# Optimization experiments

Hardware: AMD Instinct MI355X
Metric: run time of the kernel (lower is better)

## Reference

```python
import jax, jax.numpy as jnp
import numpy as np
from jax import lax

R = 3
D = (2 * R + 1) ** 2  # 49 local offsets


def _unfold(x, r):
    # torch F.unfold(kernel=2r+1, padding=r): (B,C,H,W) -> (B, C*K*K, H, W),
    # channel-major (c, ky, kx) ordering, matching conv_general_dilated_patches.
    k = 2 * r + 1
    return lax.conv_general_dilated_patches(
        x, (k, k), (1, 1), [(r, r), (r, r)],
        dimension_numbers=("NCHW", "OIHW", "NCHW"))


def _l2norm(x, eps=1e-12):
    n = jnp.sqrt(jnp.sum(x * x, axis=1, keepdims=True))
    return x / jnp.maximum(n, eps)


def setup_inputs() -> dict:
    key = jax.random.key(0)
    ks = jax.random.split(key, 8)
    B, Cin, Cmid, H, W = 2, 256, 128, 112, 112
    phi_cur = jax.random.normal(ks[0], (B, Cin, H, W), jnp.float32)
    phi_rnd = jax.random.normal(ks[1], (B, Cin, H, W), jnp.float32)
    P_cur = jax.random.normal(ks[2], (B, 3, H, W), jnp.float32)
    P_rnd = jax.random.normal(ks[3], (B, 3, H, W), jnp.float32)
    Wq = jax.random.normal(ks[4], (Cmid, Cin), jnp.float32) * 0.05
    Wk = jax.random.normal(ks[5], (Cmid, Cin), jnp.float32) * 0.05
    Wv = jax.random.normal(ks[6], (D, D), jnp.float32) * 0.1
    bv = jnp.zeros((D,), jnp.float32)
    gamma = jnp.array(1.0, jnp.float32)
    return dict(phi_cur=phi_cur, phi_rnd=phi_rnd, P_cur=P_cur, P_rnd=P_rnd,
                Wq=Wq, Wk=Wk, Wv=Wv, bv=bv, gamma=gamma)


def reference(phi_cur, phi_rnd, P_cur, P_rnd, Wq, Wk, Wv, bv, gamma):
    B, _, H, W = phi_cur.shape
    # 1x1 convs + channel L2 normalize
    q = _l2norm(jnp.einsum('oc,bchw->bohw', Wq, phi_cur))
    k = _l2norm(jnp.einsum('oc,bchw->bohw', Wk, phi_rnd))
    # local cost volume: patches (B, Cmid, D, H, W)
    patches = _unfold(k, R).reshape(B, -1, D, H, W)
    corr = jnp.einsum('bchw,bcdhw->bdhw', q, patches)  # (B,D,H,W)
    vol_corr = jnp.einsum('ed,bdhw->behw', Wv, corr) + bv[None, :, None, None]
    # geometric bias
    Pr = _unfold(P_rnd, R).reshape(B, 3, D, H, W)
    dP = P_cur[:, :, None, :, :] - Pr  # (B,3,D,H,W)
    dz = dP[:, 2]
    dist = jnp.sqrt(jnp.clip(jnp.sum(dP * dP, axis=1), 1e-12, None))
    logits = vol_corr + gamma * (-dist - 0.5 * jnp.abs(dz))
    w = jax.nn.softmax(logits, axis=1)
    off = jnp.arange(-R, R + 1, dtype=w.dtype)
    dY, dX = jnp.meshgrid(off, off, indexing='ij')
    offx = dX.reshape(1, D, 1, 1)
    offy = dY.reshape(1, D, 1, 1)
    du = jnp.sum(w * offx, axis=1, keepdims=True)
    dv = jnp.sum(w * offy, axis=1, keepdims=True)
    conf = jnp.max(w, axis=1, keepdims=True)
    return du, dv, conf
```

## Files before the change

### kernel.cpp

```cpp
#include <hip/hip_runtime.h>
#include <hip/hip_bf16.h>
#include <math.h>

constexpr int B    = 2;
constexpr int CIN  = 256;
constexpr int CMID = 128;
constexpr int H    = 112;
constexpr int W    = 112;
constexpr int HW   = H * W;
constexpr int NPIX = B * HW;
constexpr int RAD  = 3;
constexpr int KS   = 7;
constexpr int DD   = 49;

typedef __attribute__((ext_vector_type(8))) short  short8;
typedef __attribute__((ext_vector_type(4))) float  float4v;

__device__ __forceinline__ unsigned pkbf(float a, float b) {
    __hip_bfloat162 h = __float22bfloat162_rn(make_float2(a, b));
    union { __hip_bfloat162 h2; unsigned u; } c;
    c.h2 = h;
    return c.u;
}

__global__ __launch_bounds__(256) void prep(
    const float* __restrict__ Wq, const float* __restrict__ Wk,
    const float* __restrict__ Wv,
    unsigned short* __restrict__ wqb, unsigned short* __restrict__ wkb,
    float* __restrict__ wvp)
{
    if (blockIdx.x < 64) {
        const int i  = blockIdx.x * 256 + threadIdx.x;
        const int n4 = (CMID * CIN) / 4;
        const float4 v = (i < n4) ? ((const float4*)Wq)[i] : ((const float4*)Wk)[i - n4];
        uint2 r;
        r.x = pkbf(v.x, v.y);
        r.y = pkbf(v.z, v.w);
        if (i < n4) ((uint2*)wqb)[i] = r;
        else        ((uint2*)wkb)[i - n4] = r;
    } else {
        for (int idx = threadIdx.x; idx < DD * 52; idx += 256) {
            const int r = idx / 52, c = idx % 52;
            wvp[idx] = (c < DD) ? Wv[r * DD + c] : 0.f;
        }
    }
}

constexpr int PSTR = 264;

__global__ __launch_bounds__(256, 4) void proj_mfma(
    const float* __restrict__ phi_cur, const float* __restrict__ phi_rnd,
    const unsigned short* __restrict__ wq_bf, const unsigned short* __restrict__ wk_bf,
    unsigned short* __restrict__ q_ws, unsigned short* __restrict__ k_ws)
{
    __shared__ unsigned short pt[64 * PSTR];
    __shared__ float red[4][64];

    const int tid  = threadIdx.x;
    const int lane = tid & 63;
    const int wv   = __builtin_amdgcn_readfirstlane(tid >> 6);
    const int t    = blockIdx.y;

    const float* __restrict__ phi          = t ? phi_rnd : phi_cur;
    const unsigned short* __restrict__ Wbf = t ? wk_bf : wq_bf;
    unsigned short* __restrict__ outp      = t ? k_ws : q_ws;

    const int pgb = blockIdx.x * 64;
    const int b   = pgb / HW;
    const int pim = pgb % HW;
    const float* pbase = phi + (size_t)b * CIN * HW + pim;

    const int m = lane & 15, quad = lane >> 4;

    short8 af[2][8];
#pragma unroll
    for (int ot = 0; ot < 2; ++ot)
#pragma unroll
        for (int kc = 0; kc < 8; ++kc)
            af[ot][kc] = *(const short8*)(Wbf +
                (size_t)(wv * 32 + ot * 16 + m) * CIN + kc * 32 + quad * 8);

#pragma unroll
    for (int half = 0; half < 2; ++half) {
        float4 va[4], vb[4];
#pragma unroll
        for (int p = 0; p < 4; ++p) {
            const int idx = (half * 4 + p) * 256 + tid;
            const int cp  = idx >> 4;
            const int pq  = idx & 15;
            const int c0  = cp * 2;
            va[p] = *(const float4*)(pbase + (size_t)c0 * HW + pq * 4);
            vb[p] = *(const float4*)(pbase + (size_t)(c0 + 1) * HW + pq * 4);
        }
#pragma unroll
        for (int p = 0; p < 4; ++p) {
            const int idx = (half * 4 + p) * 256 + tid;
            const int cp  = idx >> 4;
            const int pq  = idx & 15;
            const int c0  = cp * 2;
            const int swz = ((pq >> 1) & 3) << 3;
            const int col = c0 ^ swz;
            *(unsigned*)(pt + (pq * 4 + 0) * PSTR + col) = pkbf(va[p].x, vb[p].x);
            *(unsigned*)(pt + (pq * 4 + 1) * PSTR + col) = pkbf(va[p].y, vb[p].y);
            *(unsigned*)(pt + (pq * 4 + 2) * PSTR + col) = pkbf(va[p].z, vb[p].z);
            *(unsigned*)(pt + (pq * 4 + 3) * PSTR + col) = pkbf(va[p].w, vb[p].w);
        }
    }

    __syncthreads();

    float4v acc[2][4];
#pragma unroll
    for (int ot = 0; ot < 2; ++ot)
#pragma unroll
        for (int nt = 0; nt < 4; ++nt) acc[ot][nt] = (float4v)0.f;

#pragma unroll
    for (int kc = 0; kc < 8; ++kc) {
        short8 bfr[4];
#pragma unroll
        for (int nt = 0; nt < 4; ++nt) {
            const int row = nt * 16 + m;
            const int col = (kc * 32 + quad * 8) ^ (((row >> 3) & 3) << 3);
            bfr[nt] = *(const short8*)(pt + row * PSTR + col);
        }
#pragma unroll
        for (int nt = 0; nt < 4; ++nt) {
            acc[0][nt] = __builtin_amdgcn_mfma_f32_16x16x32_bf16(af[0][kc], bfr[nt], acc[0][nt], 0, 0, 0);
            acc[1][nt] = __builtin_amdgcn_mfma_f32_16x16x32_bf16(af[1][kc], bfr[nt], acc[1][nt], 0, 0, 0);
        }
    }

#pragma unroll
    for (int nt = 0; nt < 4; ++nt) {
        float ss = 0.f;
#pragma unroll
        for (int ot = 0; ot < 2; ++ot)
#pragma unroll
            for (int r = 0; r < 4; ++r)
                ss = fmaf(acc[ot][nt][r], acc[ot][nt][r], ss);
        ss += __shfl_xor(ss, 16, 64);
        ss += __shfl_xor(ss, 32, 64);
        if (quad == 0) red[wv][nt * 16 + m] = ss;
    }
    __syncthreads();

    float inv[4];
#pragma unroll
    for (int nt = 0; nt < 4; ++nt) {
        const int px = nt * 16 + m;
        const float tot = red[0][px] + red[1][px] + red[2][px] + red[3][px];
        inv[nt] = 1.f / fmaxf(sqrtf(tot), 1e-12f);
    }

#pragma unroll
    for (int nt = 0; nt < 4; ++nt)
#pragma unroll
        for (int ot = 0; ot < 2; ++ot) {
            uint2 st;
            st.x = pkbf(acc[ot][nt][0] * inv[nt], acc[ot][nt][1] * inv[nt]);
            st.y = pkbf(acc[ot][nt][2] * inv[nt], acc[ot][nt][3] * inv[nt]);
            *(uint2*)(outp + (size_t)(pgb + nt * 16 + m) * CMID
                      + wv * 32 + ot * 16 + quad * 4) = st;
        }
}

constexpr int TILE = 16;
constexpr int COLS = TILE + 6;
constexpr int NV   = KS * COLS;
constexpr int KSTR = 136;

__global__ __launch_bounds__(256, 3) void corr_kernel(
    const unsigned short* __restrict__ q_ws, const unsigned short* __restrict__ k_ws,
    const float* __restrict__ P_cur, const float* __restrict__ P_rnd,
    const float* __restrict__ wvp, const float* __restrict__ bv,
    const float* __restrict__ gamma_p, float* __restrict__ out)
{
    __shared__ unsigned short kt[NV * KSTR];
    __shared__ alignas(16) unsigned short qt[TILE * KSTR];
    __shared__ float cs[TILE][52];

    const int tid  = threadIdx.x;
    const int lane = tid & 63;
    const int wv   = __builtin_amdgcn_readfirstlane(tid >> 6);

    const int fid = (blockIdx.z * H + blockIdx.y) * (W / TILE) + blockIdx.x;
    const int swz = (fid & 7) * 196 + (fid >> 3);
    const int b   = swz / (H * (W / TILE));
    const int rem = swz % (H * (W / TILE));
    const int h   = rem / (W / TILE);
    const int w0  = (rem % (W / TILE)) * TILE;

    const int sub  = tid & 15;
    const int vgrp = tid >> 4;
    uint4 stv[10];
#pragma unroll
    for (int pass = 0; pass < 10; ++pass) {
        const int vi = pass * 16 + vgrp;
        uint4 v = make_uint4(0, 0, 0, 0);
        if (vi < NV) {
            const int rr = vi / COLS;
            const int cc = vi % COLS;
            const int hh = h + rr - RAD;
            const int ww = w0 + cc - RAD;
            if (hh >= 0 && hh < H && ww >= 0 && ww < W)
                v = *(const uint4*)(k_ws + (size_t)(b * HW + hh * W + ww) * CMID + sub * 8);
        }
        stv[pass] = v;
    }
    const uint4 qv = *(const uint4*)(q_ws + (size_t)(b * HW + h * W + w0 + vgrp) * CMID + sub * 8);

    const int  ld    = (lane < DD) ? lane : 0;
    const bool valid = (lane < DD);
    float4 wq4[13];
#pragma unroll
    for (int j = 0; j < 13; ++j)
        wq4[j] = *(const float4*)(wvp + ld * 52 + j * 4);
    const float bvv   = bv[ld];
    const float gamma = gamma_p[0];

    const int dy = ld / KS - RAD;
    const int dx = ld % KS - RAD;
    float geo[4];
#pragma unroll
    for (int i = 0; i < 4; ++i) {
        const int pl = wv * 4 + i;
        const int hn = h + dy, wn = w0 + pl + dx;
        const bool inb = valid && hn >= 0 && hn < H && wn >= 0 && wn < W;
        const float* pc = P_cur + (size_t)b * 3 * HW + (h * W + w0 + pl);
        const float cx = pc[0], cy = pc[HW], cz = pc[2 * HW];
        float rx = 0.f, ry = 0.f, rz = 0.f;
        if (inb) {
            const float* pr = P_rnd + (size_t)b * 3 * HW + (hn * W + wn);
            rx = pr[0]; ry = pr[HW]; rz = pr[2 * HW];
        }
        const float dpx = cx - rx, dpy = cy - ry, dpz = cz - rz;
        const float dist = sqrtf(fmaxf(dpx * dpx + dpy * dpy + dpz * dpz, 1e-12f));
        geo[i] = gamma * (-dist - 0.5f * fabsf(dpz));
    }

#pragma unroll
    for (int pass = 0; pass < 10; ++pass) {
        const int vi = pass * 16 + vgrp;
        if (vi < NV)
            *(uint4*)(kt + vi * KSTR + sub * 8) = stv[pass];
    }
    *(uint4*)(qt + vgrp * KSTR + sub * 8) = qv;

    __syncthreads();

    if (tid < TILE * 3)
        cs[tid / 3][49 + tid % 3] = 0.f;

    const int m = lane & 15, quad = lane >> 4;
    short8 aqf[4];
#pragma unroll
    for (int kc = 0; kc < 4; ++kc)
        aqf[kc] = *(const short8*)(qt + m * KSTR + kc * 32 + quad * 8);

    for (int g = wv; g < 14; g += 4) {
        const int r  = g >> 1;
        const int nt = g & 1;
        const int vi = min(r * COLS + nt * 16 + m, NV - 1);
        const short8 b0 = *(const short8*)(kt + vi * KSTR + 0 * 32 + quad * 8);
        const short8 b1 = *(const short8*)(kt + vi * KSTR + 1 * 32 + quad * 8);
        const short8 b2 = *(const short8*)(kt + vi * KSTR + 2 * 32 + quad * 8);
        const short8 b3 = *(const short8*)(kt + vi * KSTR + 3 * 32 + quad * 8);
        float4v a0 = (float4v)0.f, a1 = (float4v)0.f;
        a0 = __builtin_amdgcn_mfma_f32_16x16x32_bf16(aqf[0], b0, a0, 0, 0, 0);
        a1 = __builtin_amdgcn_mfma_f32_16x16x32_bf16(aqf[1], b1, a1, 0, 0, 0);
        a0 = __builtin_amdgcn_mfma_f32_16x16x32_bf16(aqf[2], b2, a0, 0, 0, 0);
        a1 = __builtin_amdgcn_mfma_f32_16x16x32_bf16(aqf[3], b3, a1, 0, 0, 0);
#pragma unroll
        for (int r4 = 0; r4 < 4; ++r4) a0[r4] += a1[r4];
#pragma unroll
        for (int reg = 0; reg < 4; ++reg) {
            const int p   = quad * 4 + reg;
            const int off = nt * 16 + m - p;
            if (off >= 0 && off <= 6)
                cs[p][r * 7 + off] = a0[reg];
        }
    }
    __syncthreads();
    float* lsf = reinterpret_cast<float*>(qt);

#pragma unroll
    for (int i = 0; i < 4; ++i) {
        const int pl = wv * 4 + i;
        float logit = -INFINITY;
        if (valid) {
            float va0 = bvv, va1 = 0.f;
#pragma unroll
            for (int e4 = 0; e4 < 13; ++e4) {
                const float4 c4 = *(const float4*)&cs[pl][e4 * 4];
                const float4 w4 = wq4[e4];
                if (e4 & 1) {
                    va1 = fmaf(w4.x, c4.x, va1);
                    va1 = fmaf(w4.y, c4.y, va1);
                    va1 = fmaf(w4.z, c4.z, va1);
                    va1 = fmaf(w4.w, c4.w, va1);
                } else {
                    va0 = fmaf(w4.x, c4.x, va0);
                    va0 = fmaf(w4.y, c4.y, va0);
                    va0 = fmaf(w4.z, c4.z, va0);
                    va0 = fmaf(w4.w, c4.w, va0);
                }
            }
            logit = (va0 + va1) + geo[i];
        }
        lsf[pl * 64 + lane] = logit;
    }

    {
        const int pli = lane >> 4;
        const int dq  = lane & 15;
        const int pl  = wv * 4 + pli;

        const float4 v = ((const float4*)lsf)[pl * 16 + dq];

        float m4 = fmaxf(fmaxf(v.x, v.y), fmaxf(v.z, v.w));
#pragma unroll
        for (int s = 1; s < 16; s <<= 1)
            m4 = fmaxf(m4, __shfl_xor(m4, s, 64));

        const float e0 = __expf(v.x - m4);
        const float e1 = __expf(v.y - m4);
        const float e2 = __expf(v.z - m4);
        const float e3 = __expf(v.w - m4);
        float Z = (e0 + e1) + (e2 + e3);

        const int c0i = dq * 4;
        float dus = 0.f, dvs = 0.f;
        {
            const float ex[4] = { e0, e1, e2, e3 };
#pragma unroll
            for (int j = 0; j < 4; ++j) {
                const int col = c0i + j;
                dus = fmaf(ex[j], (float)(col % KS - RAD), dus);
                dvs = fmaf(ex[j], (float)(col / KS - RAD), dvs);
            }
        }
#pragma unroll
        for (int s = 1; s < 16; s <<= 1) {
            Z   += __shfl_xor(Z,   s, 64);
            dus += __shfl_xor(dus, s, 64);
            dvs += __shfl_xor(dvs, s, 64);
        }

        if (dq == 0) {
            const int pg = b * HW + h * W + w0 + pl;
            const float invZ = 1.f / Z;
            out[pg]            = dus * invZ;
            out[NPIX + pg]     = dvs * invZ;
            out[2 * NPIX + pg] = invZ;
        }
    }
}

extern "C" void kernel_launch(void* const* d_in, const int* in_sizes, int n_in,
                              void* d_out, int out_size, void* d_ws, size_t ws_size,
                              hipStream_t stream)
{
    const float* phi_cur = (const float*)d_in[0];
    const float* phi_rnd = (const float*)d_in[1];
    const float* P_cur   = (const float*)d_in[2];
    const float* P_rnd   = (const float*)d_in[3];
    const float* Wq      = (const float*)d_in[4];
    const float* Wk      = (const float*)d_in[5];
    const float* Wv      = (const float*)d_in[6];
    const float* bv      = (const float*)d_in[7];
    const float* gm      = (const float*)d_in[8];
    float* out = (float*)d_out;

    unsigned short* ws   = (unsigned short*)d_ws;
    unsigned short* q_ws = ws;
    unsigned short* k_ws = q_ws + (size_t)NPIX * CMID;
    unsigned short* wqb  = k_ws + (size_t)NPIX * CMID;
    unsigned short* wkb  = wqb + (size_t)CMID * CIN;
    float*          wvp  = (float*)(wkb + (size_t)CMID * CIN);

    prep<<<dim3(65), 256, 0, stream>>>(Wq, Wk, Wv, wqb, wkb, wvp);

    proj_mfma<<<dim3(NPIX / 64, 2), 256, 0, stream>>>(
        phi_cur, phi_rnd, wqb, wkb, q_ws, k_ws);

    corr_kernel<<<dim3(W / TILE, H, B), 256, 0, stream>>>(
        q_ws, k_ws, P_cur, P_rnd, wvp, bv, gm, out);
}
```

Baseline: 131.4 us.

## Split projection work by pixel rows per wave to drop block barriers

Each wave now owns 16 pixels across all 128 output channels, loading and transposing only its own pixel rows into shared memory. The L2-norm reduction can then stay inside the wave, which removes both __syncthreads and the shared reduction buffer. Weight fragments are streamed from global memory per k-chunk with a one-step software prefetch instead of being held in registers up front. The cost is that every wave re-reads the whole weight matrix, which raises global and L2 traffic.

```diff
diff --git a/kernel.cpp b/kernel.cpp
--- a/kernel.cpp
+++ b/kernel.cpp
@@ -54,7 +54,6 @@
     unsigned short* __restrict__ q_ws, unsigned short* __restrict__ k_ws)
 {
     __shared__ unsigned short pt[64 * PSTR];
-    __shared__ float red[4][64];
 
     const int tid  = threadIdx.x;
     const int lane = tid & 63;
@@ -71,98 +70,80 @@
     const float* pbase = phi + (size_t)b * CIN * HW + pim;
 
     const int m = lane & 15, quad = lane >> 4;
-
-    short8 af[2][8];
-#pragma unroll
-    for (int ot = 0; ot < 2; ++ot)
-#pragma unroll
-        for (int kc = 0; kc < 8; ++kc)
-            af[ot][kc] = *(const short8*)(Wbf +
-                (size_t)(wv * 32 + ot * 16 + m) * CIN + kc * 32 + quad * 8);
+    const int prow0 = wv * 16;
+
+    const int cpl = lane >> 2;
+    const int pq  = lane & 3;
+    const float* pb2 = pbase + prow0 + pq * 4;
 
 #pragma unroll
     for (int half = 0; half < 2; ++half) {
         float4 va[4], vb[4];
 #pragma unroll
         for (int p = 0; p < 4; ++p) {
-            const int idx = (half * 4 + p) * 256 + tid;
-            const int cp  = idx >> 4;
-            const int pq  = idx & 15;
-            const int c0  = cp * 2;
-            va[p] = *(const float4*)(pbase + (size_t)c0 * HW + pq * 4);
-            vb[p] = *(const float4*)(pbase + (size_t)(c0 + 1) * HW + pq * 4);
+            const int c0 = ((half * 4 + p) * 16 + cpl) * 2;
+            va[p] = *(const float4*)(pb2 + (size_t)c0 * HW);
+            vb[p] = *(const float4*)(pb2 + (size_t)(c0 + 1) * HW);
         }
 #pragma unroll
         for (int p = 0; p < 4; ++p) {
-            const int idx = (half * 4 + p) * 256 + tid;
-            const int cp  = idx >> 4;
-            const int pq  = idx & 15;
-            const int c0  = cp * 2;
-            const int swz = ((pq >> 1) & 3) << 3;
-            const int col = c0 ^ swz;
-            *(unsigned*)(pt + (pq * 4 + 0) * PSTR + col) = pkbf(va[p].x, vb[p].x);
-            *(unsigned*)(pt + (pq * 4 + 1) * PSTR + col) = pkbf(va[p].y, vb[p].y);
-            *(unsigned*)(pt + (pq * 4 + 2) * PSTR + col) = pkbf(va[p].z, vb[p].z);
-            *(unsigned*)(pt + (pq * 4 + 3) * PSTR + col) = pkbf(va[p].w, vb[p].w);
-        }
-    }
-
-    __syncthreads();
-
-    float4v acc[2][4];
-#pragma unroll
-    for (int ot = 0; ot < 2; ++ot)
-#pragma unroll
-        for (int nt = 0; nt < 4; ++nt) acc[ot][nt] = (float4v)0.f;
+            const int c0 = ((half * 4 + p) * 16 + cpl) * 2;
+#pragma unroll
+            for (int j = 0; j < 4; ++j) {
+                const int row = prow0 + pq * 4 + j;
+                const int col = c0 ^ (((row >> 3) & 3) << 3);
+                *(unsigned*)(pt + row * PSTR + col) =
+                    pkbf((&va[p].x)[j], (&vb[p].x)[j]);
+            }
+        }
+    }
+
+    const unsigned short* wrow = Wbf + (size_t)m * CIN + quad * 8;
+    const int brow = prow0 + m;
+    const int bswz = ((brow >> 3) & 3) << 3;
+
+    float4v acc[8];
+#pragma unroll
+    for (int ot = 0; ot < 8; ++ot) acc[ot] = (float4v)0.f;
+
+    short8 afC[8], afN[8];
+#pragma unroll
+    for (int ot = 0; ot < 8; ++ot)
+        afC[ot] = *(const short8*)(wrow + (size_t)ot * 16 * CIN);
 
 #pragma unroll
     for (int kc = 0; kc < 8; ++kc) {
-        short8 bfr[4];
-#pragma unroll
-        for (int nt = 0; nt < 4; ++nt) {
-            const int row = nt * 16 + m;
-            const int col = (kc * 32 + quad * 8) ^ (((row >> 3) & 3) << 3);
-            bfr[nt] = *(const short8*)(pt + row * PSTR + col);
-        }
-#pragma unroll
-        for (int nt = 0; nt < 4; ++nt) {
-            acc[0][nt] = __builtin_amdgcn_mfma_f32_16x16x32_bf16(af[0][kc], bfr[nt], acc[0][nt], 0, 0, 0);
-            acc[1][nt] = __builtin_amdgcn_mfma_f32_16x16x32_bf16(af[1][kc], bfr[nt], acc[1][nt], 0, 0, 0);
-        }
-    }
-
-#pragma unroll
-    for (int nt = 0; nt < 4; ++nt) {
-        float ss = 0.f;
-#pragma unroll
-        for (int ot = 0; ot < 2; ++ot)
-#pragma unroll
-            for (int r = 0; r < 4; ++r)
-                ss = fmaf(acc[ot][nt][r], acc[ot][nt][r], ss);
-        ss += __shfl_xor(ss, 16, 64);
-        ss += __shfl_xor(ss, 32, 64);
-        if (quad == 0) red[wv][nt * 16 + m] = ss;
-    }
-    __syncthreads();
-
-    float inv[4];
-#pragma unroll
-    for (int nt = 0; nt < 4; ++nt) {
-        const int px = nt * 16 + m;
-        const float tot = red[0][px] + red[1][px] + red[2][px] + red[3][px];
-        inv[nt] = 1.f / fmaxf(sqrtf(tot), 1e-12f);
-    }
-
-#pragma unroll
-    for (int nt = 0; nt < 4; ++nt)
-#pragma unroll
-        for (int ot = 0; ot < 2; ++ot) {
-            uint2 st;
-            st.x = pkbf(acc[ot][nt][0] * inv[nt], acc[ot][nt][1] * inv[nt]);
-            st.y = pkbf(acc[ot][nt][2] * inv[nt], acc[ot][nt][3] * inv[nt]);
-            *(uint2*)(outp + (size_t)(pgb + nt * 16 + m) * CMID
-                      + wv * 32 + ot * 16 + quad * 4) = st;
-        }
+        const int kn = (kc < 7) ? kc + 1 : 7;
+#pragma unroll
+        for (int ot = 0; ot < 8; ++ot)
+            afN[ot] = *(const short8*)(wrow + (size_t)ot * 16 * CIN + kn * 32);
+
+        const short8 bf = *(const short8*)(pt + brow * PSTR
+                                           + ((kc * 32 + quad * 8) ^ bswz));
+#pragma unroll
+        for (int ot = 0; ot < 8; ++ot)
+            acc[ot] = __builtin_amdgcn_mfma_f32_16x16x32_bf16(afC[ot], bf, acc[ot], 0, 0, 0);
+#pragma unroll
+        for (int ot = 0; ot < 8; ++ot) afC[ot] = afN[ot];
+    }
+
+    float ss = 0.f;
+#pragma unroll
+    for (int ot = 0; ot < 8; ++ot)
+#pragma unroll
+        for (int r = 0; r < 4; ++r)
+            ss = fmaf(acc[ot][r], acc[ot][r], ss);
+    ss += __shfl_xor(ss, 16, 64);
+    ss += __shfl_xor(ss, 32, 64);
+    const float inv = 1.f / fmaxf(sqrtf(ss), 1e-12f);
+
+#pragma unroll
+    for (int ot = 0; ot < 8; ++ot) {
+        uint2 st;
+        st.x = pkbf(acc[ot][0] * inv, acc[ot][1] * inv);
+        st.y = pkbf(acc[ot][2] * inv, acc[ot][3] * inv);
+        *(uint2*)(outp + (size_t)(pgb + prow0 + m) * CMID + ot * 16 + quad * 4) = st;
+    }
 }
 
 constexpr int TILE = 16;
```

Result: slower. 151.2 us (+15.1%).
